# Kernel optimization log

Measured on AMD Instinct MI355X. Metric: run time of the kernel, lower is better.

Reference implementation:

```python
import jax, jax.numpy as jnp
import numpy as np

# Config from module init / global Args
H = 8        # n_head
DK = 64      # d_k
DV = 64      # d_v
D = 512      # d_model
KSZ = 3      # kernel_size (args.kernel_size)
B_PARAM = 0.001
CUR_HEAD = 3
ALPHA_C = -float(np.log(B_PARAM / (H - 1) * CUR_HEAD))  # alpha_c (nonzero head)
EPS = 1e-6


def setup_inputs() -> dict:
    key = jax.random.key(0)
    ks = jax.random.split(key, 8)
    B, L = 2, 2048
    q = jax.random.normal(ks[0], (B, L, D), jnp.float32)
    k = jax.random.normal(ks[1], (B, L, D), jnp.float32)
    v = jax.random.normal(ks[2], (B, L, D), jnp.float32)
    # Linear weights stored torch-style: [out_features, in_features]
    w_q = jax.random.normal(ks[3], (H * DK, D), jnp.float32) * 0.02
    w_k = jax.random.normal(ks[4], (H * DK, D), jnp.float32) * 0.02
    w_v = jax.random.normal(ks[5], (H * DV, D), jnp.float32) * 0.02
    w_fc = jax.random.normal(ks[6], (D, H * DV), jnp.float32) * 0.02
    gamma = jnp.ones((D,), jnp.float32)
    beta = jnp.zeros((D,), jnp.float32)
    return {"q": q, "k": k, "v": v, "w_q": w_q, "w_k": w_k, "w_v": w_v,
            "w_fc": w_fc, "gamma": gamma, "beta": beta}


def reference(q, k, v, w_q, w_k, w_v, w_fc, gamma, beta):
    B, L, _ = q.shape
    residual = q
    # QKV projections -> [B, H, L, d]
    qh = jnp.einsum('bld,ed->ble', q, w_q).reshape(B, L, H, DK).transpose(0, 2, 1, 3)
    kh = jnp.einsum('bld,ed->ble', k, w_k).reshape(B, L, H, DK).transpose(0, 2, 1, 3)
    vh = jnp.einsum('bld,ed->ble', v, w_v).reshape(B, L, H, DV).transpose(0, 2, 1, 3)
    # Scores: matmul(q / sqrt(d_k), k^T)  (LaSAttention receives d_k = d_k**0.5)
    attn = jnp.einsum('bhqd,bhkd->bhqk', qh, kh) / jnp.sqrt(jnp.float32(DK))
    # Distance weighting: eld = alpha_c * -(x - y) * attn, d_l[i,j] = j - i
    idx = jnp.arange(L)
    d_l = idx[None, :] - idx[:, None]                      # [L, L]
    eld_mat = (-ALPHA_C * d_l).astype(attn.dtype)
    eld = eld_mat[None, None, :, :] * attn
    # Softmax then avg_pool1d(kernel=KSZ, stride=1, pad=(KSZ-1)//2, count_include_pad)
    p = jax.nn.softmax(eld, axis=-1)                       # [B, H, L, L]
    pad = (KSZ - 1) // 2
    pp = jnp.pad(p, ((0, 0), (0, 0), (0, 0), (pad, pad)))
    pooled = sum(pp[..., j:j + L] for j in range(KSZ)) / jnp.float32(KSZ)
    # Value matmul (seq lengths equal so no trimming needed)
    out = jnp.einsum('bhqk,bhkd->bhqd', pooled, vh)
    out = out.transpose(0, 2, 1, 3).reshape(B, L, H * DV)
    # Output projection (dropout is identity in eval), residual, LayerNorm
    out = jnp.einsum('ble,de->bld', out, w_fc)
    out = out[:, :, None, :] + residual[:, :, None, :]     # [B, L, 1, D]
    mu = out.mean(axis=-1, keepdims=True)
    var = ((out - mu) ** 2).mean(axis=-1, keepdims=True)
    out = (out - mu) / jnp.sqrt(var + EPS) * gamma + beta
    return (out, pooled)
```

## Files before the change

### kernel.cpp

```cpp
#include <hip/hip_runtime.h>
#include <cstddef>
#include <cstdint>

#define ALPHA_C 7.7550531393693407f
constexpr int BB = 2;
constexpr int LL = 2048;
constexpr int HH = 8;
constexpr size_t OUT0  = (size_t)BB * LL * 512;
constexpr size_t PLANE = (size_t)BB * HH * LL * 64;
constexpr size_t XN    = (size_t)BB * LL * 512;
constexpr size_t WN    = (size_t)512 * 512;

typedef __attribute__((ext_vector_type(8))) short bf16x8;
typedef __attribute__((ext_vector_type(4))) short short4v;
typedef __attribute__((ext_vector_type(4))) float f32x4;

__device__ inline short f2bf(float x) {
  union { float f; unsigned u; } un; un.f = x;
  unsigned r = un.u + 0x7fffu + ((un.u >> 16) & 1u);
  return (short)(r >> 16);
}
__device__ inline float bf2f(short s) {
  union { unsigned u; float f; } un; un.u = ((unsigned)(unsigned short)s) << 16;
  return un.f;
}
__device__ inline void split3(float x, short& h, short& m, short& l) {
  h = f2bf(x); float r = x - bf2f(h);
  m = f2bf(r); float r2 = r - bf2f(m);
  l = f2bf(r2);
}

__global__ __launch_bounds__(256) void k_split3x(
    const float* __restrict__ a, const float* __restrict__ b, const float* __restrict__ c,
    short* __restrict__ da, short* __restrict__ db, short* __restrict__ dc, size_t n)
{
  size_t i = ((size_t)blockIdx.x * 256 + threadIdx.x) * 4;
  if (i >= n) return;
  const float* srcs[3] = {a, b, c};
  short* dsts[3] = {da, db, dc};
  #pragma unroll
  for (int s = 0; s < 3; ++s) {
    float4 x = *(const float4*)&srcs[s][i];
    short4v h, m, l;
    short th, tm, tl;
    split3(x.x, th, tm, tl); h[0] = th; m[0] = tm; l[0] = tl;
    split3(x.y, th, tm, tl); h[1] = th; m[1] = tm; l[1] = tl;
    split3(x.z, th, tm, tl); h[2] = th; m[2] = tm; l[2] = tl;
    split3(x.w, th, tm, tl); h[3] = th; m[3] = tm; l[3] = tl;
    *(short4v*)&dsts[s][i]         = h;
    *(short4v*)&dsts[s][n + i]     = m;
    *(short4v*)&dsts[s][2 * n + i] = l;
  }
}

__global__ __launch_bounds__(256) void k_vavg(
    const short* __restrict__ vt, short* __restrict__ vavgt)
{
  const size_t row = blockIdx.x;
  const short* src = vt + row * LL;
  short* dst = vavgt + row * LL;
  const int c0 = threadIdx.x * 8;
  bf16x8 x = *(const bf16x8*)&src[c0];
  float xf[10];
  xf[0] = (c0 > 0) ? bf2f(src[c0 - 1]) : 0.f;
  #pragma unroll
  for (int i = 0; i < 8; ++i) xf[i + 1] = bf2f(x[i]);
  xf[9] = (c0 + 8 < LL) ? bf2f(src[c0 + 8]) : 0.f;
  bf16x8 o;
  #pragma unroll
  for (int i = 0; i < 8; ++i) o[i] = f2bf((xf[i] + xf[i + 1] + xf[i + 2]) * (1.0f / 3.0f));
  *(bf16x8*)&dst[c0] = o;
}

__global__ __launch_bounds__(256) void k_proj(
    const short* __restrict__ xq, const short* __restrict__ xk, const short* __restrict__ xv,
    const short* __restrict__ wq3, const short* __restrict__ wk3, const short* __restrict__ wv3,
    short* __restrict__ qs, short* __restrict__ ks, short* __restrict__ vt)
{
  const int bx  = blockIdx.x;
  const int sel = bx >> 3;
  const int n0  = (bx & 7) * 64;
  const int m0  = blockIdx.y * 64;
  const short* X = sel == 0 ? xq  : (sel == 1 ? xk  : xv);
  const short* W = sel == 0 ? wq3 : (sel == 1 ? wk3 : wv3);

  __shared__ short Xs[3][64 * 72];
  __shared__ short Ws[3][64 * 72];
  const int tid = threadIdx.x;
  const int lane = tid & 63, w = tid >> 6;
  const int quad = lane >> 4, l15 = lane & 15, colg = l15;
  const int sr8 = tid >> 3, sc8 = (tid & 7) * 8;

  f32x4 acc[4];
  #pragma unroll
  for (int t = 0; t < 4; ++t) { acc[t][0]=0.f; acc[t][1]=0.f; acc[t][2]=0.f; acc[t][3]=0.f; }

  for (int kt = 0; kt < 8; ++kt) {
    const int k0 = kt * 64;
    #pragma unroll
    for (int p = 0; p < 3; ++p) {
      #pragma unroll
      for (int it = 0; it < 2; ++it) {
        int r = it * 32 + sr8;
        *(bf16x8*)&Xs[p][r * 72 + sc8] = *(const bf16x8*)&X[p * XN + (size_t)(m0 + r) * 512 + k0 + sc8];
        *(bf16x8*)&Ws[p][r * 72 + sc8] = *(const bf16x8*)&W[p * WN + (size_t)(n0 + r) * 512 + k0 + sc8];
      }
    }
    __syncthreads();
    #pragma unroll
    for (int ch = 0; ch < 2; ++ch) {
      const int ka = (quad << 3) + ch * 32;
      const int ar = (w * 16 + l15) * 72 + ka;
      bf16x8 ah = *(const bf16x8*)&Xs[0][ar];
      bf16x8 am = *(const bf16x8*)&Xs[1][ar];
      bf16x8 al = *(const bf16x8*)&Xs[2][ar];
      #pragma unroll
      for (int t = 0; t < 4; ++t) {
        const int br = (t * 16 + l15) * 72 + ka;
        bf16x8 bh_ = *(const bf16x8*)&Ws[0][br];
        bf16x8 bm_ = *(const bf16x8*)&Ws[1][br];
        bf16x8 bl_ = *(const bf16x8*)&Ws[2][br];
        acc[t] = __builtin_amdgcn_mfma_f32_16x16x32_bf16(ah, bh_, acc[t], 0, 0, 0);
        acc[t] = __builtin_amdgcn_mfma_f32_16x16x32_bf16(ah, bm_, acc[t], 0, 0, 0);
        acc[t] = __builtin_amdgcn_mfma_f32_16x16x32_bf16(am, bh_, acc[t], 0, 0, 0);
        acc[t] = __builtin_amdgcn_mfma_f32_16x16x32_bf16(ah, bl_, acc[t], 0, 0, 0);
        acc[t] = __builtin_amdgcn_mfma_f32_16x16x32_bf16(al, bh_, acc[t], 0, 0, 0);
        acc[t] = __builtin_amdgcn_mfma_f32_16x16x32_bf16(am, bm_, acc[t], 0, 0, 0);
      }
    }
    __syncthreads();
  }

  if (sel < 2) {
    short* Y = sel == 0 ? qs : ks;
    #pragma unroll
    for (int t = 0; t < 4; ++t) {
      const int e = n0 + t * 16 + colg, h = e >> 6, dk = e & 63;
      #pragma unroll
      for (int r = 0; r < 4; ++r) {
        const int m = m0 + w * 16 + quad * 4 + r;
        const int b = m >> 11, l = m & 2047;
        size_t base = ((size_t)(b * HH + h) * LL + l) * 64 + dk;
        short hh, mm, ll; split3(acc[t][r], hh, mm, ll);
        Y[base] = hh; Y[PLANE + base] = mm; Y[2 * PLANE + base] = ll;
      }
    }
  } else {
    const int b  = m0 >> 11;
    const int l0 = (m0 & 2047) + w * 16 + quad * 4;
    #pragma unroll
    for (int t = 0; t < 4; ++t) {
      const int e = n0 + t * 16 + colg, h = e >> 6, dk = e & 63;
      short4v s;
      #pragma unroll
      for (int r = 0; r < 4; ++r) s[r] = f2bf(acc[t][r]);
      *(short4v*)&vt[(((size_t)b * HH + h) * 64 + dk) * LL + l0] = s;
    }
  }
}

__global__ __launch_bounds__(256) void k_stats(
    const short* __restrict__ qs, const short* __restrict__ ks,
    float* __restrict__ rowstats)
{
  const int i0 = blockIdx.x * 64;
  const int bh = blockIdx.y;
  __shared__ short Ks[3][64 * 72];
  const int tid = threadIdx.x;
  const int lane = tid & 63, w = tid >> 6;
  const int quad = lane >> 4, colg = lane & 15, l15 = lane & 15;
  const int sr8 = tid >> 3, sc8 = (tid & 7) * 8;

  bf16x8 qf[3][2];
  {
    const size_t qoff = ((size_t)bh * LL + i0 + w * 16 + l15) * 64 + (quad << 3);
    #pragma unroll
    for (int p = 0; p < 3; ++p)
      #pragma unroll
      for (int ch = 0; ch < 2; ++ch)
        qf[p][ch] = *(const bf16x8*)&qs[p * PLANE + qoff + ch * 32];
  }

  const short* kbase = ks + (size_t)bh * LL * 64;
  #pragma unroll
  for (int p = 0; p < 3; ++p)
    #pragma unroll
    for (int it = 0; it < 2; ++it) {
      int r = it * 32 + sr8;
      *(bf16x8*)&Ks[p][r * 72 + sc8] = *(const bf16x8*)&kbase[p * PLANE + (size_t)r * 64 + sc8];
    }
  __syncthreads();

  float M[4], S[4];
  #pragma unroll
  for (int r = 0; r < 4; ++r) { M[r] = -3.0e38f; S[r] = 0.f; }

  for (int jt = 0; jt < 32; ++jt) {
    const int j0 = jt * 64;
    bf16x8 kreg[3][2];
    if (jt + 1 < 32) {
      #pragma unroll
      for (int p = 0; p < 3; ++p)
        #pragma unroll
        for (int it = 0; it < 2; ++it) {
          int r = it * 32 + sr8;
          kreg[p][it] = *(const bf16x8*)&kbase[p * PLANE + ((size_t)(jt + 1) * 64 + r) * 64 + sc8];
        }
    }

    f32x4 acc[4];
    #pragma unroll
    for (int t = 0; t < 4; ++t) { acc[t][0]=0.f; acc[t][1]=0.f; acc[t][2]=0.f; acc[t][3]=0.f; }
    #pragma unroll
    for (int ch = 0; ch < 2; ++ch) {
      const int ka = (quad << 3) + ch * 32;
      #pragma unroll
      for (int t = 0; t < 4; ++t) {
        const int br = (t * 16 + l15) * 72 + ka;
        bf16x8 bh_ = *(const bf16x8*)&Ks[0][br];
        bf16x8 bm_ = *(const bf16x8*)&Ks[1][br];
        bf16x8 bl_ = *(const bf16x8*)&Ks[2][br];
        acc[t] = __builtin_amdgcn_mfma_f32_16x16x32_bf16(qf[0][ch], bh_, acc[t], 0, 0, 0);
        acc[t] = __builtin_amdgcn_mfma_f32_16x16x32_bf16(qf[0][ch], bm_, acc[t], 0, 0, 0);
        acc[t] = __builtin_amdgcn_mfma_f32_16x16x32_bf16(qf[1][ch], bh_, acc[t], 0, 0, 0);
        acc[t] = __builtin_amdgcn_mfma_f32_16x16x32_bf16(qf[0][ch], bl_, acc[t], 0, 0, 0);
        acc[t] = __builtin_amdgcn_mfma_f32_16x16x32_bf16(qf[2][ch], bh_, acc[t], 0, 0, 0);
        acc[t] = __builtin_amdgcn_mfma_f32_16x16x32_bf16(qf[1][ch], bm_, acc[t], 0, 0, 0);
      }
    }

    #pragma unroll
    for (int r = 0; r < 4; ++r) {
      const int irow = i0 + w * 16 + quad * 4 + r;
      float e0 = -ALPHA_C * (float)(j0 +  0 + colg - irow) * (acc[0][r] * 0.125f);
      float e1 = -ALPHA_C * (float)(j0 + 16 + colg - irow) * (acc[1][r] * 0.125f);
      float e2 = -ALPHA_C * (float)(j0 + 32 + colg - irow) * (acc[2][r] * 0.125f);
      float e3 = -ALPHA_C * (float)(j0 + 48 + colg - irow) * (acc[3][r] * 0.125f);
      float mx = fmaxf(fmaxf(e0, e1), fmaxf(e2, e3));
      float nM = fmaxf(M[r], mx);
      S[r] = S[r] * __expf(M[r] - nM)
           + __expf(e0 - nM) + __expf(e1 - nM) + __expf(e2 - nM) + __expf(e3 - nM);
      M[r] = nM;
    }

    __syncthreads();
    if (jt + 1 < 32) {
      #pragma unroll
      for (int p = 0; p < 3; ++p)
        #pragma unroll
        for (int it = 0; it < 2; ++it) {
          int r = it * 32 + sr8;
          *(bf16x8*)&Ks[p][r * 72 + sc8] = kreg[p][it];
        }
    }
    __syncthreads();
  }

  #pragma unroll
  for (int r = 0; r < 4; ++r) {
    float M_ = M[r], S_ = S[r];
    #pragma unroll
    for (int d = 1; d < 16; d <<= 1) {
      float Mo = __shfl_xor(M_, d);
      float So = __shfl_xor(S_, d);
      float nM = fmaxf(M_, Mo);
      S_ = S_ * __expf(M_ - nM) + So * __expf(Mo - nM);
      M_ = nM;
    }
    if (colg == 0) {
      int irow = i0 + w * 16 + quad * 4 + r;
      size_t idx = ((size_t)bh * LL + irow) * 2;
      rowstats[idx] = M_; rowstats[idx + 1] = S_;
    }
  }
}

__global__ __launch_bounds__(256) void k_pool_pv(
    const short* __restrict__ qs, const short* __restrict__ ks,
    const short* __restrict__ vavgt, const float* __restrict__ rowstats,
    float* __restrict__ pooled, float* __restrict__ outh)
{
  const int i0 = blockIdx.x * 64;
  const int bh = blockIdx.y;
  const int b = bh >> 3, h = bh & 7;
  float*       Pg = pooled + (size_t)bh * LL * LL;
  const short* Vt = vavgt + (size_t)bh * 64 * LL;
  const short* kbase = ks + (size_t)bh * LL * 64;

  __shared__ short Ks[3][64 * 72];
  __shared__ short Vsm[64 * 72];
  __shared__ short Pa[2][64 * 72];
  __shared__ float Mrow[64], invSr[64], lhalo[64];

  const int tid = threadIdx.x;
  const int lane = tid & 63, w = tid >> 6;
  const int quad = lane >> 4, colg = lane & 15, l15 = lane & 15;
  const int sr8 = tid >> 3, sc8 = (tid & 7) * 8;

  bf16x8 qf[3][2];
  {
    const size_t qoff = ((size_t)bh * LL + i0 + w * 16 + l15) * 64 + (quad << 3);
    #pragma unroll
    for (int p = 0; p < 3; ++p)
      #pragma unroll
      for (int ch = 0; ch < 2; ++ch)
        qf[p][ch] = *(const bf16x8*)&qs[p * PLANE + qoff + ch * 32];
  }
  if (tid < 64) {
    float2 ms = *(const float2*)&rowstats[((size_t)bh * LL + i0 + tid) * 2];
    Mrow[tid] = ms.x; invSr[tid] = 1.0f / ms.y; lhalo[tid] = 0.f;
  }

  #pragma unroll
  for (int p = 0; p < 3; ++p)
    #pragma unroll
    for (int it = 0; it < 2; ++it) {
      int r = it * 32 + sr8;
      *(bf16x8*)&Ks[p][r * 72 + sc8] = *(const bf16x8*)&kbase[p * PLANE + (size_t)r * 64 + sc8];
    }
  __syncthreads();

  f32x4 pv[4];
  #pragma unroll
  for (int t = 0; t < 4; ++t) { pv[t][0]=0.f; pv[t][1]=0.f; pv[t][2]=0.f; pv[t][3]=0.f; }

  for (int jt = 0; jt <= 32; ++jt) {
    if (jt < 32) {
      const int j0 = jt * 64;
      f32x4 acc[4];
      #pragma unroll
      for (int t = 0; t < 4; ++t) { acc[t][0]=0.f; acc[t][1]=0.f; acc[t][2]=0.f; acc[t][3]=0.f; }
      #pragma unroll
      for (int ch = 0; ch < 2; ++ch) {
        const int ka = (quad << 3) + ch * 32;
        #pragma unroll
        for (int t = 0; t < 4; ++t) {
          const int br = (t * 16 + l15) * 72 + ka;
          bf16x8 bh_ = *(const bf16x8*)&Ks[0][br];
          bf16x8 bm_ = *(const bf16x8*)&Ks[1][br];
          bf16x8 bl_ = *(const bf16x8*)&Ks[2][br];
          acc[t] = __builtin_amdgcn_mfma_f32_16x16x32_bf16(qf[0][ch], bh_, acc[t], 0, 0, 0);
          acc[t] = __builtin_amdgcn_mfma_f32_16x16x32_bf16(qf[0][ch], bm_, acc[t], 0, 0, 0);
          acc[t] = __builtin_amdgcn_mfma_f32_16x16x32_bf16(qf[1][ch], bh_, acc[t], 0, 0, 0);
          acc[t] = __builtin_amdgcn_mfma_f32_16x16x32_bf16(qf[0][ch], bl_, acc[t], 0, 0, 0);
          acc[t] = __builtin_amdgcn_mfma_f32_16x16x32_bf16(qf[2][ch], bh_, acc[t], 0, 0, 0);
          acc[t] = __builtin_amdgcn_mfma_f32_16x16x32_bf16(qf[1][ch], bm_, acc[t], 0, 0, 0);
        }
      }
      short* Pc = Pa[jt & 1];
      #pragma unroll
      for (int r = 0; r < 4; ++r) {
        const int row = w * 16 + quad * 4 + r;
        const int irow = i0 + row;
        const float Mr = Mrow[row], iS = invSr[row];
        #pragma unroll
        for (int t = 0; t < 4; ++t) {
          int jl = t * 16 + colg;
          float e = -ALPHA_C * (float)(j0 + jl - irow) * (acc[t][r] * 0.125f);
          Pc[row * 72 + jl] = f2bf(__expf(e - Mr) * iS);
        }
      }
    }
    if (jt >= 1) {
      #pragma unroll
      for (int it = 0; it < 2; ++it) {
        int d = it * 32 + sr8;
        *(bf16x8*)&Vsm[d * 72 + sc8] = *(const bf16x8*)&Vt[(size_t)d * LL + (jt - 1) * 64 + sc8];
      }
    }
    __syncthreads();

    if (jt >= 1) {
      const short* Pp = Pa[(jt - 1) & 1];
      const short* Pn = Pa[jt & 1];
      #pragma unroll
      for (int u = 0; u < 2; ++u) {
        const int row = (u == 0) ? (tid >> 3) : (tid >> 3) + 32;
        const int c0 = (tid & 7) * 8;
        bf16x8 x = *(const bf16x8*)&Pp[row * 72 + c0];
        float xf[8];
        #pragma unroll
        for (int i = 0; i < 8; ++i) xf[i] = bf2f(x[i]);
        float lft = (c0 == 0)  ? lhalo[row] : bf2f(Pp[row * 72 + c0 - 1]);
        float rgt = (c0 == 56) ? ((jt < 32) ? bf2f(Pn[row * 72]) : 0.f)
                               : bf2f(Pp[row * 72 + c0 + 8]);
        f32x4 o0, o1;
        o0[0] = (lft   + xf[0] + xf[1]) * (1.0f/3.0f);
        o0[1] = (xf[0] + xf[1] + xf[2]) * (1.0f/3.0f);
        o0[2] = (xf[1] + xf[2] + xf[3]) * (1.0f/3.0f);
        o0[3] = (xf[2] + xf[3] + xf[4]) * (1.0f/3.0f);
        o1[0] = (xf[3] + xf[4] + xf[5]) * (1.0f/3.0f);
        o1[1] = (xf[4] + xf[5] + xf[6]) * (1.0f/3.0f);
        o1[2] = (xf[5] + xf[6] + xf[7]) * (1.0f/3.0f);
        o1[3] = (xf[6] + xf[7] + rgt  ) * (1.0f/3.0f);
        float* dst = &Pg[(size_t)(i0 + row) * LL + (jt - 1) * 64 + c0];
        __builtin_nontemporal_store(o0, (f32x4*)dst);
        __builtin_nontemporal_store(o1, (f32x4*)(dst + 4));
        if (c0 == 56) lhalo[row] = xf[7];
      }
      #pragma unroll
      for (int ch = 0; ch < 2; ++ch) {
        const int ka = (quad << 3) + ch * 32;
        bf16x8 af = *(const bf16x8*)&Pp[(w * 16 + l15) * 72 + ka];
        #pragma unroll
        for (int t = 0; t < 4; ++t) {
          bf16x8 bfv = *(const bf16x8*)&Vsm[(t * 16 + l15) * 72 + ka];
          pv[t] = __builtin_amdgcn_mfma_f32_16x16x32_bf16(af, bfv, pv[t], 0, 0, 0);
        }
      }
    }
    if (jt + 1 < 32) {
      #pragma unroll
      for (int p = 0; p < 3; ++p)
        #pragma unroll
        for (int it = 0; it < 2; ++it) {
          int r = it * 32 + sr8;
          *(bf16x8*)&Ks[p][r * 72 + sc8] =
              *(const bf16x8*)&kbase[p * PLANE + ((size_t)(jt + 1) * 64 + r) * 64 + sc8];
        }
    }
    __syncthreads();
  }

  #pragma unroll
  for (int t = 0; t < 4; ++t)
    #pragma unroll
    for (int r = 0; r < 4; ++r) {
      int i = i0 + w * 16 + quad * 4 + r;
      int d = t * 16 + colg;
      outh[((size_t)b * LL + i) * 512 + h * 64 + d] = pv[t][r];
    }
}

__global__ __launch_bounds__(256) void k_fc(
    const float* __restrict__ outh, const float* __restrict__ wfc, float* __restrict__ fcout)
{
  const int n0 = blockIdx.x * 64;
  const int m0 = blockIdx.y * 64;
  __shared__ short Asm[64 * 72];
  __shared__ short Bsm[64 * 72];
  const int tid = threadIdx.x;
  const int lane = tid & 63, w = tid >> 6;

  f32x4 acc[4];
  #pragma unroll
  for (int t = 0; t < 4; ++t) { acc[t][0]=0.f; acc[t][1]=0.f; acc[t][2]=0.f; acc[t][3]=0.f; }

  const int sr = tid >> 6, sc = tid & 63;
  for (int k0 = 0; k0 < 512; k0 += 64) {
    #pragma unroll
    for (int it = 0; it < 16; ++it) {
      int r = it * 4 + sr;
      Asm[r*72 + sc] = f2bf(outh[(size_t)(m0 + r) * 512 + k0 + sc]);
      Bsm[r*72 + sc] = f2bf(wfc [(size_t)(n0 + r) * 512 + k0 + sc]);
    }
    __syncthreads();
    #pragma unroll
    for (int ch = 0; ch < 2; ++ch) {
      const int ka = ((lane >> 4) << 3) + ch * 32;
      bf16x8 af = *(const bf16x8*)&Asm[(w * 16 + (lane & 15)) * 72 + ka];
      #pragma unroll
      for (int t = 0; t < 4; ++t) {
        bf16x8 bfv = *(const bf16x8*)&Bsm[(t * 16 + (lane & 15)) * 72 + ka];
        acc[t] = __builtin_amdgcn_mfma_f32_16x16x32_bf16(af, bfv, acc[t], 0, 0, 0);
      }
    }
    __syncthreads();
  }
  const int q4 = lane >> 4, colg = lane & 15;
  #pragma unroll
  for (int t = 0; t < 4; ++t)
    #pragma unroll
    for (int r = 0; r < 4; ++r) {
      int m = m0 + w * 16 + q4 * 4 + r;
      fcout[(size_t)m * 512 + n0 + t * 16 + colg] = acc[t][r];
    }
}

__global__ __launch_bounds__(256) void k_ln(
    const float* __restrict__ fcout, const float* __restrict__ resid,
    const float* __restrict__ gamma, const float* __restrict__ beta,
    float* __restrict__ out)
{
  const size_t row = blockIdx.x;
  const int tid = threadIdx.x;
  __shared__ float red[256];

  float x0 = fcout[row * 512 + tid]       + resid[row * 512 + tid];
  float x1 = fcout[row * 512 + 256 + tid] + resid[row * 512 + 256 + tid];

  red[tid] = x0 + x1; __syncthreads();
  for (int off = 128; off > 0; off >>= 1) {
    if (tid < off) red[tid] += red[tid + off];
    __syncthreads();
  }
  const float mu = red[0] * (1.0f / 512.0f); __syncthreads();

  float d0 = x0 - mu, d1 = x1 - mu;
  red[tid] = d0 * d0 + d1 * d1; __syncthreads();
  for (int off = 128; off > 0; off >>= 1) {
    if (tid < off) red[tid] += red[tid + off];
    __syncthreads();
  }
  const float var = red[0] * (1.0f / 512.0f);
  const float rstd = 1.0f / sqrtf(var + 1e-6f);

  out[row * 512 + tid]       = d0 * rstd * gamma[tid]       + beta[tid];
  out[row * 512 + 256 + tid] = d1 * rstd * gamma[tid + 256] + beta[tid + 256];
}

extern "C" void kernel_launch(void* const* d_in, const int* in_sizes, int n_in,
                              void* d_out, int out_size, void* d_ws, size_t ws_size,
                              hipStream_t stream)
{
  const float* q     = (const float*)d_in[0];
  const float* k     = (const float*)d_in[1];
  const float* v     = (const float*)d_in[2];
  const float* wq    = (const float*)d_in[3];
  const float* wk    = (const float*)d_in[4];
  const float* wv    = (const float*)d_in[5];
  const float* wfc   = (const float*)d_in[6];
  const float* gamma = (const float*)d_in[7];
  const float* beta  = (const float*)d_in[8];

  float* out    = (float*)d_out;
  float* pooled = out + OUT0;

  short* xq    = (short*)d_ws;
  short* xk    = xq + 3 * XN;
  short* xv    = xk + 3 * XN;
  short* wq3   = xv + 3 * XN;
  short* wk3   = wq3 + 3 * WN;
  short* wv3   = wk3 + 3 * WN;
  short* qsp   = wv3 + 3 * WN;
  short* ksp   = qsp + 3 * PLANE;
  short* vt    = ksp + 3 * PLANE;
  short* vavgt = vt + PLANE;
  float* outh     = (float*)(vavgt + PLANE);
  float* rowstats = outh + OUT0;
  float* fcout    = rowstats + 2 * (size_t)BB * HH * LL;

  k_split3x<<<dim3((unsigned)(XN / 4 / 256)), 256, 0, stream>>>(q, k, v, xq, xk, xv, XN);
  k_split3x<<<dim3((unsigned)(WN / 4 / 256)), 256, 0, stream>>>(wq, wk, wv, wq3, wk3, wv3, WN);
  k_proj   <<<dim3(24, 64), 256, 0, stream>>>(xq, xk, xv, wq3, wk3, wv3, qsp, ksp, vt);
  k_vavg   <<<dim3(1024),   256, 0, stream>>>(vt, vavgt);
  k_stats  <<<dim3(32, 16), 256, 0, stream>>>(qsp, ksp, rowstats);
  k_pool_pv<<<dim3(32, 16), 256, 0, stream>>>(qsp, ksp, vavgt, rowstats, pooled, outh);
  k_fc     <<<dim3(8, 64),  256, 0, stream>>>(outh, wfc, fcout);
  k_ln     <<<dim3(4096),   256, 0, stream>>>(fcout, q, gamma, beta, out);
}
```

Before: 562.2 us.

## Store per-tile exponentials from stats pass to skip QK recompute in PV pass

The stats kernel now writes bf16 exponentials for each 64x64 tile, along with a per-tile row max, to a global buffer. The pool/PV kernel rescales those stored values using the final row stats, so it no longer recomputes QK^T with six split-precision MFMAs. This removes half of the QK matmul work but adds a 128 MB write and read of intermediate values, and each exponential is rounded to bf16 twice. The fc input is also switched to bf16 (outh and a pre-converted w_fc) with vectorized loads.

Result: no change. 573.0 us (+1.9%).

```diff
diff --git a/kernel.cpp b/kernel.cpp
--- a/kernel.cpp
+++ b/kernel.cpp
@@ -10,6 +10,7 @@
 constexpr size_t PLANE = (size_t)BB * HH * LL * 64;
 constexpr size_t XN    = (size_t)BB * LL * 512;
 constexpr size_t WN    = (size_t)512 * 512;
+constexpr size_t UN    = (size_t)16 * 32 * 32 * 4096;
 
 typedef __attribute__((ext_vector_type(8))) short bf16x8;
 typedef __attribute__((ext_vector_type(4))) short short4v;
@@ -53,6 +54,19 @@
   }
 }
 
+__global__ __launch_bounds__(256) void k_cvtbf(
+    const float* __restrict__ src, short* __restrict__ dst, size_t n)
+{
+  size_t i = ((size_t)blockIdx.x * 256 + threadIdx.x) * 8;
+  if (i >= n) return;
+  float4 a = *(const float4*)&src[i];
+  float4 b = *(const float4*)&src[i + 4];
+  bf16x8 o;
+  o[0] = f2bf(a.x); o[1] = f2bf(a.y); o[2] = f2bf(a.z); o[3] = f2bf(a.w);
+  o[4] = f2bf(b.x); o[5] = f2bf(b.y); o[6] = f2bf(b.z); o[7] = f2bf(b.w);
+  *(bf16x8*)&dst[i] = o;
+}
+
 __global__ __launch_bounds__(256) void k_vavg(
     const short* __restrict__ vt, short* __restrict__ vavgt)
 {
@@ -159,13 +173,14 @@
   }
 }
 
-__global__ __launch_bounds__(256) void k_stats(
+__global__ __launch_bounds__(256) void k_qk_exp(
     const short* __restrict__ qs, const short* __restrict__ ks,
-    float* __restrict__ rowstats)
+    short* __restrict__ u_g, float* __restrict__ mstats, float* __restrict__ rowstats)
 {
   const int i0 = blockIdx.x * 64;
   const int bh = blockIdx.y;
   __shared__ short Ks[3][64 * 72];
+  __shared__ short Us[64 * 72];
   const int tid = threadIdx.x;
   const int lane = tid & 63, w = tid >> 6;
   const int quad = lane >> 4, colg = lane & 15, l15 = lane & 15;
@@ -231,19 +246,31 @@
 
     #pragma unroll
     for (int r = 0; r < 4; ++r) {
-      const int irow = i0 + w * 16 + quad * 4 + r;
+      const int row = w * 16 + quad * 4 + r;
+      const int irow = i0 + row;
       float e0 = -ALPHA_C * (float)(j0 +  0 + colg - irow) * (acc[0][r] * 0.125f);
       float e1 = -ALPHA_C * (float)(j0 + 16 + colg - irow) * (acc[1][r] * 0.125f);
       float e2 = -ALPHA_C * (float)(j0 + 32 + colg - irow) * (acc[2][r] * 0.125f);
       float e3 = -ALPHA_C * (float)(j0 + 48 + colg - irow) * (acc[3][r] * 0.125f);
       float mx = fmaxf(fmaxf(e0, e1), fmaxf(e2, e3));
+      #pragma unroll
+      for (int d = 1; d < 16; d <<= 1) mx = fmaxf(mx, __shfl_xor(mx, d));
+      float u0 = __expf(e0 - mx), u1 = __expf(e1 - mx);
+      float u2 = __expf(e2 - mx), u3 = __expf(e3 - mx);
+      float s = u0 + u1 + u2 + u3;
+      #pragma unroll
+      for (int d = 1; d < 16; d <<= 1) s += __shfl_xor(s, d);
       float nM = fmaxf(M[r], mx);
-      S[r] = S[r] * __expf(M[r] - nM)
-           + __expf(e0 - nM) + __expf(e1 - nM) + __expf(e2 - nM) + __expf(e3 - nM);
+      S[r] = S[r] * __expf(M[r] - nM) + s * __expf(mx - nM);
       M[r] = nM;
-    }
-
-    __syncthreads();
+      Us[row * 72 +  0 + colg] = f2bf(u0);
+      Us[row * 72 + 16 + colg] = f2bf(u1);
+      Us[row * 72 + 32 + colg] = f2bf(u2);
+      Us[row * 72 + 48 + colg] = f2bf(u3);
+      if (colg == 0) mstats[((size_t)bh * 32 + jt) * LL + irow] = mx;
+    }
+    __syncthreads();
+
     if (jt + 1 < 32) {
       #pragma unroll
       for (int p = 0; p < 3; ++p)
@@ -253,71 +280,56 @@
           *(bf16x8*)&Ks[p][r * 72 + sc8] = kreg[p][it];
         }
     }
-    __syncthreads();
-  }
-
-  #pragma unroll
-  for (int r = 0; r < 4; ++r) {
-    float M_ = M[r], S_ = S[r];
-    #pragma unroll
-    for (int d = 1; d < 16; d <<= 1) {
-      float Mo = __shfl_xor(M_, d);
-      float So = __shfl_xor(S_, d);
-      float nM = fmaxf(M_, Mo);
-      S_ = S_ * __expf(M_ - nM) + So * __expf(Mo - nM);
-      M_ = nM;
-    }
-    if (colg == 0) {
+    {
+      const size_t ubase = (((size_t)bh * 32 + blockIdx.x) * 32 + jt) * 4096;
+      #pragma unroll
+      for (int it = 0; it < 2; ++it) {
+        int rr = it * 32 + sr8;
+        bf16x8 uu = *(const bf16x8*)&Us[rr * 72 + sc8];
+        *(bf16x8*)&u_g[ubase + (size_t)rr * 64 + sc8] = uu;
+      }
+    }
+    __syncthreads();
+  }
+
+  if (colg == 0) {
+    #pragma unroll
+    for (int r = 0; r < 4; ++r) {
       int irow = i0 + w * 16 + quad * 4 + r;
       size_t idx = ((size_t)bh * LL + irow) * 2;
-      rowstats[idx] = M_; rowstats[idx + 1] = S_;
-    }
-  }
-}
-
-__global__ __launch_bounds__(256) void k_pool_pv(
-    const short* __restrict__ qs, const short* __restrict__ ks,
+      rowstats[idx] = M[r]; rowstats[idx + 1] = S[r];
+    }
+  }
+}
+
+__global__ __launch_bounds__(256) void k_pv2(
+    const short* __restrict__ u_g, const float* __restrict__ mstats,
     const short* __restrict__ vavgt, const float* __restrict__ rowstats,
-    float* __restrict__ pooled, float* __restrict__ outh)
-{
-  const int i0 = blockIdx.x * 64;
+    float* __restrict__ pooled, short* __restrict__ outh)
+{
+  const int i0 = blockIdx.x * 64, ib = blockIdx.x;
   const int bh = blockIdx.y;
   const int b = bh >> 3, h = bh & 7;
   float*       Pg = pooled + (size_t)bh * LL * LL;
   const short* Vt = vavgt + (size_t)bh * 64 * LL;
-  const short* kbase = ks + (size_t)bh * LL * 64;
-
-  __shared__ short Ks[3][64 * 72];
+
   __shared__ short Vsm[64 * 72];
   __shared__ short Pa[2][64 * 72];
-  __shared__ float Mrow[64], invSr[64], lhalo[64];
+  __shared__ float lhalo[64];
 
   const int tid = threadIdx.x;
   const int lane = tid & 63, w = tid >> 6;
   const int quad = lane >> 4, colg = lane & 15, l15 = lane & 15;
   const int sr8 = tid >> 3, sc8 = (tid & 7) * 8;
 
-  bf16x8 qf[3][2];
+  const int r0 = sr8, r1 = sr8 + 32;
+  float M0, iS0, M1, iS1;
   {
-    const size_t qoff = ((size_t)bh * LL + i0 + w * 16 + l15) * 64 + (quad << 3);
-    #pragma unroll
-    for (int p = 0; p < 3; ++p)
-      #pragma unroll
-      for (int ch = 0; ch < 2; ++ch)
-        qf[p][ch] = *(const bf16x8*)&qs[p * PLANE + qoff + ch * 32];
-  }
-  if (tid < 64) {
-    float2 ms = *(const float2*)&rowstats[((size_t)bh * LL + i0 + tid) * 2];
-    Mrow[tid] = ms.x; invSr[tid] = 1.0f / ms.y; lhalo[tid] = 0.f;
-  }
-
-  #pragma unroll
-  for (int p = 0; p < 3; ++p)
-    #pragma unroll
-    for (int it = 0; it < 2; ++it) {
-      int r = it * 32 + sr8;
-      *(bf16x8*)&Ks[p][r * 72 + sc8] = *(const bf16x8*)&kbase[p * PLANE + (size_t)r * 64 + sc8];
-    }
+    float2 a = *(const float2*)&rowstats[((size_t)bh * LL + i0 + r0) * 2];
+    float2 c = *(const float2*)&rowstats[((size_t)bh * LL + i0 + r1) * 2];
+    M0 = a.x; iS0 = 1.0f / a.y; M1 = c.x; iS1 = 1.0f / c.y;
+  }
+  if (tid < 64) lhalo[tid] = 0.f;
   __syncthreads();
 
   f32x4 pv[4];
@@ -326,40 +338,20 @@
 
   for (int jt = 0; jt <= 32; ++jt) {
     if (jt < 32) {
-      const int j0 = jt * 64;
-      f32x4 acc[4];
-      #pragma unroll
-      for (int t = 0; t < 4; ++t) { acc[t][0]=0.f; acc[t][1]=0.f; acc[t][2]=0.f; acc[t][3]=0.f; }
-      #pragma unroll
-      for (int ch = 0; ch < 2; ++ch) {
-        const int ka = (quad << 3) + ch * 32;
-        #pragma unroll
-        for (int t = 0; t < 4; ++t) {
-          const int br = (t * 16 + l15) * 72 + ka;
-          bf16x8 bh_ = *(const bf16x8*)&Ks[0][br];
-          bf16x8 bm_ = *(const bf16x8*)&Ks[1][br];
-          bf16x8 bl_ = *(const bf16x8*)&Ks[2][br];
-          acc[t] = __builtin_amdgcn_mfma_f32_16x16x32_bf16(qf[0][ch], bh_, acc[t], 0, 0, 0);
-          acc[t] = __builtin_amdgcn_mfma_f32_16x16x32_bf16(qf[0][ch], bm_, acc[t], 0, 0, 0);
-          acc[t] = __builtin_amdgcn_mfma_f32_16x16x32_bf16(qf[1][ch], bh_, acc[t], 0, 0, 0);
-          acc[t] = __builtin_amdgcn_mfma_f32_16x16x32_bf16(qf[0][ch], bl_, acc[t], 0, 0, 0);
-          acc[t] = __builtin_amdgcn_mfma_f32_16x16x32_bf16(qf[2][ch], bh_, acc[t], 0, 0, 0);
-          acc[t] = __builtin_amdgcn_mfma_f32_16x16x32_bf16(qf[1][ch], bm_, acc[t], 0, 0, 0);
-        }
-      }
-      short* Pc = Pa[jt & 1];
-      #pragma unroll
-      for (int r = 0; r < 4; ++r) {
-        const int row = w * 16 + quad * 4 + r;
-        const int irow = i0 + row;
-        const float Mr = Mrow[row], iS = invSr[row];
-        #pragma unroll
-        for (int t = 0; t < 4; ++t) {
-          int jl = t * 16 + colg;
-          float e = -ALPHA_C * (float)(j0 + jl - irow) * (acc[t][r] * 0.125f);
-          Pc[row * 72 + jl] = f2bf(__expf(e - Mr) * iS);
-        }
-      }
+      const size_t ubase = (((size_t)bh * 32 + ib) * 32 + jt) * 4096;
+      const float* mst = &mstats[((size_t)bh * 32 + jt) * LL + i0];
+      float c0 = __expf(mst[r0] - M0) * iS0;
+      float c1 = __expf(mst[r1] - M1) * iS1;
+      bf16x8 u0 = *(const bf16x8*)&u_g[ubase + (size_t)r0 * 64 + sc8];
+      bf16x8 u1 = *(const bf16x8*)&u_g[ubase + (size_t)r1 * 64 + sc8];
+      bf16x8 p0, p1;
+      #pragma unroll
+      for (int i = 0; i < 8; ++i) {
+        p0[i] = f2bf(bf2f(u0[i]) * c0);
+        p1[i] = f2bf(bf2f(u1[i]) * c1);
+      }
+      *(bf16x8*)&Pa[jt & 1][r0 * 72 + sc8] = p0;
+      *(bf16x8*)&Pa[jt & 1][r1 * 72 + sc8] = p1;
     }
     if (jt >= 1) {
       #pragma unroll
@@ -409,16 +401,6 @@
         }
       }
     }
-    if (jt + 1 < 32) {
-      #pragma unroll
-      for (int p = 0; p < 3; ++p)
-        #pragma unroll
-        for (int it = 0; it < 2; ++it) {
-          int r = it * 32 + sr8;
-          *(bf16x8*)&Ks[p][r * 72 + sc8] =
-              *(const bf16x8*)&kbase[p * PLANE + ((size_t)(jt + 1) * 64 + r) * 64 + sc8];
-        }
-    }
     __syncthreads();
   }
 
@@ -428,12 +410,12 @@
     for (int r = 0; r < 4; ++r) {
       int i = i0 + w * 16 + quad * 4 + r;
       int d = t * 16 + colg;
-      outh[((size_t)b * LL + i) * 512 + h * 64 + d] = pv[t][r];
+      outh[((size_t)b * LL + i) * 512 + h * 64 + d] = f2bf(pv[t][r]);
     }
 }
 
 __global__ __launch_bounds__(256) void k_fc(
-    const float* __restrict__ outh, const float* __restrict__ wfc, float* __restrict__ fcout)
+    const short* __restrict__ outh, const short* __restrict__ wfcb, float* __restrict__ fcout)
 {
   const int n0 = blockIdx.x * 64;
   const int m0 = blockIdx.y * 64;
@@ -441,18 +423,18 @@
   __shared__ short Bsm[64 * 72];
   const int tid = threadIdx.x;
   const int lane = tid & 63, w = tid >> 6;
+  const int sr8 = tid >> 3, sc8 = (tid & 7) * 8;
 
   f32x4 acc[4];
   #pragma unroll
   for (int t = 0; t < 4; ++t) { acc[t][0]=0.f; acc[t][1]=0.f; acc[t][2]=0.f; acc[t][3]=0.f; }
 
-  const int sr = tid >> 6, sc = tid & 63;
   for (int k0 = 0; k0 < 512; k0 += 64) {
     #pragma unroll
-    for (int it = 0; it < 16; ++it) {
-      int r = it * 4 + sr;
-      Asm[r*72 + sc] = f2bf(outh[(size_t)(m0 + r) * 512 + k0 + sc]);
-      Bsm[r*72 + sc] = f2bf(wfc [(size_t)(n0 + r) * 512 + k0 + sc]);
+    for (int it = 0; it < 2; ++it) {
+      int r = it * 32 + sr8;
+      *(bf16x8*)&Asm[r * 72 + sc8] = *(const bf16x8*)&outh[(size_t)(m0 + r) * 512 + k0 + sc8];
+      *(bf16x8*)&Bsm[r * 72 + sc8] = *(const bf16x8*)&wfcb[(size_t)(n0 + r) * 512 + k0 + sc8];
     }
     __syncthreads();
     #pragma unroll
@@ -536,16 +518,20 @@
   short* ksp   = qsp + 3 * PLANE;
   short* vt    = ksp + 3 * PLANE;
   short* vavgt = vt + PLANE;
-  float* outh     = (float*)(vavgt + PLANE);
-  float* rowstats = outh + OUT0;
+  short* wfcb  = vavgt + PLANE;
+  short* outh  = wfcb + WN;
+  short* u_g   = outh + OUT0;
+  float* mstats   = (float*)(u_g + UN);
+  float* rowstats = mstats + (size_t)16 * 32 * LL;
   float* fcout    = rowstats + 2 * (size_t)BB * HH * LL;
 
   k_split3x<<<dim3((unsigned)(XN / 4 / 256)), 256, 0, stream>>>(q, k, v, xq, xk, xv, XN);
   k_split3x<<<dim3((unsigned)(WN / 4 / 256)), 256, 0, stream>>>(wq, wk, wv, wq3, wk3, wv3, WN);
+  k_cvtbf  <<<dim3((unsigned)(WN / 8 / 256)), 256, 0, stream>>>(wfc, wfcb, WN);
   k_proj   <<<dim3(24, 64), 256, 0, stream>>>(xq, xk, xv, wq3, wk3, wv3, qsp, ksp, vt);
   k_vavg   <<<dim3(1024),   256, 0, stream>>>(vt, vavgt);
-  k_stats  <<<dim3(32, 16), 256, 0, stream>>>(qsp, ksp, rowstats);
-  k_pool_pv<<<dim3(32, 16), 256, 0, stream>>>(qsp, ksp, vavgt, rowstats, pooled, outh);
-  k_fc     <<<dim3(8, 64),  256, 0, stream>>>(outh, wfc, fcout);
+  k_qk_exp <<<dim3(32, 16), 256, 0, stream>>>(qsp, ksp, u_g, mstats, rowstats);
+  k_pv2    <<<dim3(32, 16), 256, 0, stream>>>(u_g, mstats, vavgt, rowstats, pooled, outh);
+  k_fc     <<<dim3(8, 64),  256, 0, stream>>>(outh, wfcb, fcout);
   k_ln     <<<dim3(4096),   256, 0, stream>>>(fcout, q, gamma, beta, out);
 }
```

## Split softmax row-stats over key halves and feed bf16 into output projection

Applied to the files above, without the earlier changes.

The row max/sum pass now splits the key dimension into two halves across a new grid dimension. This doubles the number of blocks (512 to 1024), and a small merge kernel combines the partial max/sum pairs. Separately, the attention output is stored as bf16 and w_fc is pre-converted to bf16, so the FC GEMM loads with 16-byte vector reads instead of scalar fp32 loads plus conversion. This adds two small kernel launches and an extra partial-stats buffer. It also rounds the attention output earlier, which matches what the GEMM already did.

After: 507.3 us. -9.8%, faster.

```diff
diff --git a/kernel.cpp b/kernel.cpp
--- a/kernel.cpp
+++ b/kernel.cpp
@@ -53,6 +53,19 @@
   }
 }
 
+__global__ __launch_bounds__(256) void k_cvtbf(
+    const float* __restrict__ src, short* __restrict__ dst, size_t n)
+{
+  size_t i = ((size_t)blockIdx.x * 256 + threadIdx.x) * 8;
+  if (i >= n) return;
+  float4 a = *(const float4*)&src[i];
+  float4 b = *(const float4*)&src[i + 4];
+  bf16x8 o;
+  o[0] = f2bf(a.x); o[1] = f2bf(a.y); o[2] = f2bf(a.z); o[3] = f2bf(a.w);
+  o[4] = f2bf(b.x); o[5] = f2bf(b.y); o[6] = f2bf(b.z); o[7] = f2bf(b.w);
+  *(bf16x8*)&dst[i] = o;
+}
+
 __global__ __launch_bounds__(256) void k_vavg(
     const short* __restrict__ vt, short* __restrict__ vavgt)
 {
@@ -161,10 +174,11 @@
 
 __global__ __launch_bounds__(256) void k_stats(
     const short* __restrict__ qs, const short* __restrict__ ks,
-    float* __restrict__ rowstats)
+    float* __restrict__ statspart)
 {
   const int i0 = blockIdx.x * 64;
-  const int bh = blockIdx.y;
+  const int jh = blockIdx.y;
+  const int bh = blockIdx.z;
   __shared__ short Ks[3][64 * 72];
   const int tid = threadIdx.x;
   const int lane = tid & 63, w = tid >> 6;
@@ -181,13 +195,15 @@
         qf[p][ch] = *(const bf16x8*)&qs[p * PLANE + qoff + ch * 32];
   }
 
+  const int jt0 = jh * 16;
   const short* kbase = ks + (size_t)bh * LL * 64;
   #pragma unroll
   for (int p = 0; p < 3; ++p)
     #pragma unroll
     for (int it = 0; it < 2; ++it) {
       int r = it * 32 + sr8;
-      *(bf16x8*)&Ks[p][r * 72 + sc8] = *(const bf16x8*)&kbase[p * PLANE + (size_t)r * 64 + sc8];
+      *(bf16x8*)&Ks[p][r * 72 + sc8] =
+          *(const bf16x8*)&kbase[p * PLANE + ((size_t)jt0 * 64 + r) * 64 + sc8];
     }
   __syncthreads();
 
@@ -195,10 +211,11 @@
   #pragma unroll
   for (int r = 0; r < 4; ++r) { M[r] = -3.0e38f; S[r] = 0.f; }
 
-  for (int jt = 0; jt < 32; ++jt) {
+  for (int jj = 0; jj < 16; ++jj) {
+    const int jt = jt0 + jj;
     const int j0 = jt * 64;
     bf16x8 kreg[3][2];
-    if (jt + 1 < 32) {
+    if (jj + 1 < 16) {
       #pragma unroll
       for (int p = 0; p < 3; ++p)
         #pragma unroll
@@ -244,7 +261,7 @@
     }
 
     __syncthreads();
-    if (jt + 1 < 32) {
+    if (jj + 1 < 16) {
       #pragma unroll
       for (int p = 0; p < 3; ++p)
         #pragma unroll
@@ -269,16 +286,27 @@
     }
     if (colg == 0) {
       int irow = i0 + w * 16 + quad * 4 + r;
-      size_t idx = ((size_t)bh * LL + irow) * 2;
-      rowstats[idx] = M_; rowstats[idx + 1] = S_;
-    }
-  }
+      size_t idx = (((size_t)jh * 16 + bh) * LL + irow) * 2;
+      statspart[idx] = M_; statspart[idx + 1] = S_;
+    }
+  }
+}
+
+__global__ __launch_bounds__(256) void k_mergestats(
+    const float* __restrict__ statspart, float* __restrict__ rowstats)
+{
+  const size_t row = (size_t)blockIdx.x * 256 + threadIdx.x;
+  float2 a = *(const float2*)&statspart[row * 2];
+  float2 b = *(const float2*)&statspart[(size_t)16 * LL * 2 + row * 2];
+  float nM = fmaxf(a.x, b.x);
+  float S = a.y * __expf(a.x - nM) + b.y * __expf(b.x - nM);
+  rowstats[row * 2] = nM; rowstats[row * 2 + 1] = S;
 }
 
 __global__ __launch_bounds__(256) void k_pool_pv(
     const short* __restrict__ qs, const short* __restrict__ ks,
     const short* __restrict__ vavgt, const float* __restrict__ rowstats,
-    float* __restrict__ pooled, float* __restrict__ outh)
+    float* __restrict__ pooled, short* __restrict__ outh)
 {
   const int i0 = blockIdx.x * 64;
   const int bh = blockIdx.y;
@@ -428,12 +456,12 @@
     for (int r = 0; r < 4; ++r) {
       int i = i0 + w * 16 + quad * 4 + r;
       int d = t * 16 + colg;
-      outh[((size_t)b * LL + i) * 512 + h * 64 + d] = pv[t][r];
+      outh[((size_t)b * LL + i) * 512 + h * 64 + d] = f2bf(pv[t][r]);
     }
 }
 
 __global__ __launch_bounds__(256) void k_fc(
-    const float* __restrict__ outh, const float* __restrict__ wfc, float* __restrict__ fcout)
+    const short* __restrict__ outh, const short* __restrict__ wfcb, float* __restrict__ fcout)
 {
   const int n0 = blockIdx.x * 64;
   const int m0 = blockIdx.y * 64;
@@ -441,18 +469,18 @@
   __shared__ short Bsm[64 * 72];
   const int tid = threadIdx.x;
   const int lane = tid & 63, w = tid >> 6;
+  const int sr8 = tid >> 3, sc8 = (tid & 7) * 8;
 
   f32x4 acc[4];
   #pragma unroll
   for (int t = 0; t < 4; ++t) { acc[t][0]=0.f; acc[t][1]=0.f; acc[t][2]=0.f; acc[t][3]=0.f; }
 
-  const int sr = tid >> 6, sc = tid & 63;
   for (int k0 = 0; k0 < 512; k0 += 64) {
     #pragma unroll
-    for (int it = 0; it < 16; ++it) {
-      int r = it * 4 + sr;
-      Asm[r*72 + sc] = f2bf(outh[(size_t)(m0 + r) * 512 + k0 + sc]);
-      Bsm[r*72 + sc] = f2bf(wfc [(size_t)(n0 + r) * 512 + k0 + sc]);
+    for (int it = 0; it < 2; ++it) {
+      int r = it * 32 + sr8;
+      *(bf16x8*)&Asm[r * 72 + sc8] = *(const bf16x8*)&outh[(size_t)(m0 + r) * 512 + k0 + sc8];
+      *(bf16x8*)&Bsm[r * 72 + sc8] = *(const bf16x8*)&wfcb[(size_t)(n0 + r) * 512 + k0 + sc8];
     }
     __syncthreads();
     #pragma unroll
@@ -536,16 +564,20 @@
   short* ksp   = qsp + 3 * PLANE;
   short* vt    = ksp + 3 * PLANE;
   short* vavgt = vt + PLANE;
-  float* outh     = (float*)(vavgt + PLANE);
-  float* rowstats = outh + OUT0;
-  float* fcout    = rowstats + 2 * (size_t)BB * HH * LL;
+  short* wfcb  = vavgt + PLANE;
+  short* outh  = wfcb + WN;
+  float* statspart = (float*)(outh + OUT0);
+  float* rowstats  = statspart + 4 * (size_t)BB * HH * LL;
+  float* fcout     = rowstats + 2 * (size_t)BB * HH * LL;
 
   k_split3x<<<dim3((unsigned)(XN / 4 / 256)), 256, 0, stream>>>(q, k, v, xq, xk, xv, XN);
   k_split3x<<<dim3((unsigned)(WN / 4 / 256)), 256, 0, stream>>>(wq, wk, wv, wq3, wk3, wv3, WN);
+  k_cvtbf  <<<dim3((unsigned)(WN / 8 / 256)), 256, 0, stream>>>(wfc, wfcb, WN);
   k_proj   <<<dim3(24, 64), 256, 0, stream>>>(xq, xk, xv, wq3, wk3, wv3, qsp, ksp, vt);
   k_vavg   <<<dim3(1024),   256, 0, stream>>>(vt, vavgt);
-  k_stats  <<<dim3(32, 16), 256, 0, stream>>>(qsp, ksp, rowstats);
+  k_stats  <<<dim3(32, 2, 16), 256, 0, stream>>>(qsp, ksp, statspart);
+  k_mergestats<<<dim3(128), 256, 0, stream>>>(statspart, rowstats);
   k_pool_pv<<<dim3(32, 16), 256, 0, stream>>>(qsp, ksp, vavgt, rowstats, pooled, outh);
-  k_fc     <<<dim3(8, 64),  256, 0, stream>>>(outh, wfc, fcout);
+  k_fc     <<<dim3(8, 64),  256, 0, stream>>>(outh, wfcb, fcout);
   k_ln     <<<dim3(4096),   256, 0, stream>>>(fcout, q, gamma, beta, out);
 }
```
